# Kernel optimization log

Hardware: AMD Instinct MI355X
Metric: run time of the kernel (lower is better)

The kernel has to match this reference:

```python
import jax, jax.numpy as jnp
import numpy as np

N = 262144      # total nodes
G = 256         # graphs
P = 1024        # nodes per graph (k=None sort pool keeps all)
E = 4194304     # edges
F_IN = 128
H = 32
C = 10          # out capsules / classes
OUT_LEN = 16
IN_LEN = 96     # 3 * 32 concat
NUM_ITERS = 3


def setup_inputs() -> dict:
    key = jax.random.key(0)
    ks = jax.random.split(key, 12)
    x = jax.random.normal(ks[0], (N, F_IN), jnp.float32)
    # edges within each graph of size P
    src = jax.random.randint(ks[1], (E,), 0, N)
    off = jax.random.randint(ks[2], (E,), 0, P)
    dst = (src // P) * P + off
    edge_index = jnp.stack([src, dst]).astype(jnp.int64)
    batch = jnp.repeat(jnp.arange(G), P).astype(jnp.int64)
    W1 = jax.random.normal(ks[3], (F_IN, H), jnp.float32) / np.sqrt(F_IN)
    b1 = jnp.zeros((H,), jnp.float32)
    W2 = jax.random.normal(ks[4], (H, H), jnp.float32) / np.sqrt(H)
    b2 = jnp.zeros((H,), jnp.float32)
    W3 = jax.random.normal(ks[5], (H, H), jnp.float32) / np.sqrt(H)
    b3 = jnp.zeros((H,), jnp.float32)
    caps_W = jax.random.normal(ks[6], (C, OUT_LEN, IN_LEN), jnp.float32) * 0.05
    return {"x": x, "edge_index": edge_index, "batch": batch,
            "W1": W1, "b1": b1, "W2": W2, "b2": b2, "W3": W3, "b3": b3,
            "caps_W": caps_W}


def _position_encoding(length, dim):
    pos = jnp.arange(length, dtype=jnp.float32)[:, None]
    i = jnp.arange(dim // 2, dtype=jnp.float32)[None, :]
    ang = pos / jnp.power(10000.0, 2.0 * i / dim)
    return jnp.stack([jnp.sin(ang), jnp.cos(ang)], axis=-1).reshape(length, dim)


def _squash(v, eps=1e-12):
    n2 = jnp.sum(v * v, axis=-1, keepdims=True)
    return (n2 / (1.0 + n2)) * v / jnp.sqrt(n2 + eps)


def reference(x, edge_index, batch, W1, b1, W2, b2, W3, b3, caps_W):
    src, dst = edge_index[0], edge_index[1]
    # remove_self_loops, then GCNConv re-adds self loops with weight 1
    mask = (src != dst).astype(x.dtype)
    deg = jax.ops.segment_sum(mask, dst, num_segments=N) + 1.0
    dis = jax.lax.rsqrt(deg)                         # deg^{-1/2}
    enorm = dis[src] * dis[dst] * mask               # [E]

    def gcn(h, W, b):
        h = h @ W                                    # [N,H]
        agg = jax.ops.segment_sum(h[src] * enorm[:, None], dst, num_segments=N)
        agg = agg + h * (dis * dis)[:, None]         # self-loop term deg^{-1}
        return jnp.tanh(agg + b)

    x1 = gcn(x, W1, b1)
    x2 = gcn(x1, W2, b2)
    x3 = gcn(x2, W3, b3)
    h = jnp.concatenate([x1, x2, x3], axis=-1)       # [N, 96]

    # global_sort_pool (k=None): per-graph sort by last channel, descending
    hg = h.reshape(G, P, IN_LEN)
    order = jnp.argsort(-hg[:, :, -1], axis=1)
    hs = jnp.take_along_axis(hg, order[:, :, None], axis=1)  # [G,P,96]
    hs = hs + _position_encoding(P, IN_LEN)[None]

    # CapsuleLinear, shared weight: priors [G, C, P, OUT_LEN]
    priors = jnp.einsum('oji,gki->gokj', caps_W, hs)

    # k-means routing
    v = jnp.mean(priors, axis=2, keepdims=True)      # [G,C,1,OUT_LEN]
    for _ in range(NUM_ITERS):
        vn = v / (jnp.linalg.norm(v, axis=-1, keepdims=True) + 1e-12)
        logits = jnp.sum(priors * vn, axis=-1, keepdims=True)  # [G,C,P,1]
        prob = jax.nn.softmax(logits, axis=2)
        v = jnp.sum(prob * priors, axis=2, keepdims=True)
    out = _squash(v)[:, :, 0, :]                     # [G, C, OUT_LEN]
    return jnp.linalg.norm(out, axis=-1)             # [G, C]
```

## Files before the change

### kernel.cpp

```cpp
#include <hip/hip_runtime.h>
#include <hip/hip_fp16.h>
#include <cstdint>
#include <cstddef>

#define N_NODES   262144
#define NG        256
#define PP        1024
#define NE        4194304
#define FIN       128
#define HH        32
#define NC        10
#define OL        16
#define IL        96
#define NITER     3
#define ECHUNK    4096
#define NCHUNK    (NE/ECHUNK)
#define ECAP      18432
#define HSTR      36

typedef _Float16 half8 __attribute__((ext_vector_type(8)));
typedef float f32x4 __attribute__((ext_vector_type(4)));

__global__ void k_hist(const int* __restrict__ ei, unsigned* __restrict__ histT) {
  __shared__ unsigned lh[NG];
  int t = threadIdx.x, b = blockIdx.x;
  lh[t] = 0;
  __syncthreads();
  int base = b * ECHUNK;
  for (int q = t; q < ECHUNK; q += 256) {
    int e = base + q;
    int s = ei[e], d = ei[NE + e];
    if (s != d) atomicAdd(&lh[s >> 10], 1u);
  }
  __syncthreads();
  histT[t * NCHUNK + b] = lh[t];
}

__global__ void k_scanA(const unsigned* __restrict__ histT, unsigned* __restrict__ cbaseT,
                        unsigned* __restrict__ gtot) {
  __shared__ unsigned wtot[4];
  int t = threadIdx.x, g = blockIdx.x;
  int lane = t & 63, wv = t >> 6;
  uint4 hv = *(const uint4*)(histT + (size_t)g * NCHUNK + t * 4);
  unsigned s0 = hv.x, s1 = s0 + hv.y, s2 = s1 + hv.z, s3 = s2 + hv.w;
  unsigned tsum = s3, sc = tsum;
  for (int d = 1; d < 64; d <<= 1) {
    unsigned v = __shfl_up(sc, d, 64);
    if (lane >= d) sc += v;
  }
  if (lane == 63) wtot[wv] = sc;
  __syncthreads();
  unsigned woff = 0;
  for (int w = 0; w < wv; ++w) woff += wtot[w];
  unsigned base = woff + sc - tsum;
  cbaseT[(size_t)(t * 4 + 0) * NG + g] = base;
  cbaseT[(size_t)(t * 4 + 1) * NG + g] = base + s0;
  cbaseT[(size_t)(t * 4 + 2) * NG + g] = base + s1;
  cbaseT[(size_t)(t * 4 + 3) * NG + g] = base + s2;
  if (t == 255) gtot[g] = woff + sc;
}

__global__ void k_scanB(const unsigned* __restrict__ gtot, unsigned* __restrict__ gbase) {
  __shared__ unsigned wtot[4];
  int t = threadIdx.x;
  int lane = t & 63, wv = t >> 6;
  unsigned x = gtot[t], sc = x;
  for (int d = 1; d < 64; d <<= 1) {
    unsigned v = __shfl_up(sc, d, 64);
    if (lane >= d) sc += v;
  }
  if (lane == 63) wtot[wv] = sc;
  __syncthreads();
  unsigned woff = 0;
  for (int w = 0; w < wv; ++w) woff += wtot[w];
  gbase[t] = woff + sc - x;
  if (t == 255) gbase[256] = woff + sc;
}

__global__ void k_scatter(const int* __restrict__ ei, const unsigned* __restrict__ cbaseT,
                          const unsigned* __restrict__ gbase, unsigned* __restrict__ epack) {
  __shared__ unsigned lcur[NG];
  int t = threadIdx.x, b = blockIdx.x;
  lcur[t] = gbase[t] + cbaseT[(size_t)b * NG + t];
  __syncthreads();
  int base = b * ECHUNK;
  for (int q = t; q < ECHUNK; q += 256) {
    int e = base + q;
    int s = ei[e], d = ei[NE + e];
    if (s != d) {
      int g = s >> 10;
      unsigned pos = atomicAdd(&lcur[g], 1u);
      epack[pos] = (unsigned)(s & 1023) | ((unsigned)(d & 1023) << 10);
    }
  }
}

__global__ __launch_bounds__(256) void k_dstsort(const unsigned* __restrict__ epack,
                          const unsigned* __restrict__ gbase,
                          unsigned short* __restrict__ esrc16,
                          unsigned* __restrict__ dstptr) {
  __shared__ unsigned shist[PP];
  __shared__ unsigned wsum[256];
  __shared__ unsigned cur[PP];
  int t = threadIdx.x, g = blockIdx.x;
  unsigned e0 = gbase[g], e1 = gbase[g + 1];
  for (int i = t; i < PP; i += 256) shist[i] = 0;
  __syncthreads();
  for (unsigned e = e0 + t; e < e1; e += 256)
    atomicAdd(&shist[(epack[e] >> 10) & 1023], 1u);
  __syncthreads();
  unsigned h0 = shist[4 * t], h1 = shist[4 * t + 1], h2 = shist[4 * t + 2], h3 = shist[4 * t + 3];
  unsigned tsum = h0 + h1 + h2 + h3;
  wsum[t] = tsum;
  __syncthreads();
  for (int off = 1; off < 256; off <<= 1) {
    unsigned v = (t >= off) ? wsum[t - off] : 0u;
    __syncthreads();
    wsum[t] += v;
    __syncthreads();
  }
  unsigned excl = wsum[t] - tsum;
  unsigned c0 = excl, c1 = c0 + h0, c2 = c1 + h1, c3 = c2 + h2;
  cur[4 * t] = c0; cur[4 * t + 1] = c1; cur[4 * t + 2] = c2; cur[4 * t + 3] = c3;
  unsigned* dp = dstptr + (size_t)g * (PP + 1);
  dp[4 * t] = c0; dp[4 * t + 1] = c1; dp[4 * t + 2] = c2; dp[4 * t + 3] = c3;
  if (t == 0) dp[PP] = e1 - e0;
  __syncthreads();
  unsigned short* eg = esrc16 + (size_t)g * ECAP;
  for (unsigned e = e0 + t; e < e1; e += 256) {
    unsigned pk = epack[e];
    unsigned so = pk & 1023, dofs = (pk >> 10) & 1023;
    unsigned pos = atomicAdd(&cur[dofs], 1u);
    if (pos < ECAP) eg[pos] = (unsigned short)so;
  }
}

__global__ void k_dis(const unsigned* __restrict__ dstptr, float* __restrict__ dis) {
  int n = blockIdx.x * 256 + threadIdx.x;
  int g = n >> 10, k = n & 1023;
  const unsigned* dp = dstptr + (size_t)g * (PP + 1) + k;
  float deg = (float)(dp[1] - dp[0]);
  dis[n] = 1.0f / sqrtf(deg + 1.0f);
}

__device__ __forceinline__ void gcn_layer(float* hsl, const float* dg, const unsigned* dp,
                                          const unsigned short* eg, const float* bias,
                                          int coloff, const float* Wn, float* hbase, int t) {
  float4 bl[8];
#pragma unroll
  for (int j = 0; j < 8; ++j) bl[j] = ((const float4*)bias)[j];
  if (Wn) {
#pragma unroll
    for (int pp = 0; pp < 8; ++pp) {
      int p = t + pp * 512;
      hsl[(p >> 2) * HSTR + 32 + (p & 3)] = Wn[p];
    }
  }
  float xn[2][32];
#pragma unroll
  for (int pth = 0; pth < 2; ++pth) {
    int k = t + pth * 512;
    float dk = dg[k];
    unsigned e0 = dp[k], e1 = dp[k + 1];
    if (e1 > (unsigned)ECAP) e1 = ECAP;
    float4 acc[8];
    const float* sp = &hsl[k * HSTR];
#pragma unroll
    for (int j = 0; j < 8; ++j) acc[j] = *(const float4*)(sp + 4 * j);
    unsigned e = e0;
    for (; e + 1 < e1; e += 2) {
      int s0 = eg[e], s1 = eg[e + 1];
      const float* q0 = &hsl[s0 * HSTR];
      const float* q1 = &hsl[s1 * HSTR];
#pragma unroll
      for (int j = 0; j < 8; ++j) {
        float4 a = *(const float4*)(q0 + 4 * j);
        float4 b2 = *(const float4*)(q1 + 4 * j);
        acc[j].x += a.x + b2.x; acc[j].y += a.y + b2.y;
        acc[j].z += a.z + b2.z; acc[j].w += a.w + b2.w;
      }
    }
    if (e < e1) {
      int s0 = eg[e];
      const float* q0 = &hsl[s0 * HSTR];
#pragma unroll
      for (int j = 0; j < 8; ++j) {
        float4 a = *(const float4*)(q0 + 4 * j);
        acc[j].x += a.x; acc[j].y += a.y; acc[j].z += a.z; acc[j].w += a.w;
      }
    }
#pragma unroll
    for (int j = 0; j < 8; ++j) {
      xn[pth][4 * j + 0] = tanhf(dk * acc[j].x + bl[j].x);
      xn[pth][4 * j + 1] = tanhf(dk * acc[j].y + bl[j].y);
      xn[pth][4 * j + 2] = tanhf(dk * acc[j].z + bl[j].z);
      xn[pth][4 * j + 3] = tanhf(dk * acc[j].w + bl[j].w);
    }
    float* hr = hbase + (size_t)k * IL + coloff;
#pragma unroll
    for (int j = 0; j < 8; ++j) {
      float4 s;
      s.x = xn[pth][4 * j]; s.y = xn[pth][4 * j + 1];
      s.z = xn[pth][4 * j + 2]; s.w = xn[pth][4 * j + 3];
      *(float4*)(hr + 4 * j) = s;
    }
  }
  __syncthreads();
  if (Wn) {
#pragma unroll
    for (int pth = 0; pth < 2; ++pth) {
      int k = t + pth * 512;
      float dk = dg[k];
      float4 o4[8];
#pragma unroll
      for (int j = 0; j < 8; ++j) { o4[j].x = 0.f; o4[j].y = 0.f; o4[j].z = 0.f; o4[j].w = 0.f; }
#pragma unroll
      for (int c = 0; c < 32; ++c) {
        float xc = xn[pth][c];
#pragma unroll
        for (int j4 = 0; j4 < 8; ++j4) {
          float4 w = *(const float4*)&hsl[(c * 8 + j4) * HSTR + 32];
          o4[j4].x += xc * w.x; o4[j4].y += xc * w.y;
          o4[j4].z += xc * w.z; o4[j4].w += xc * w.w;
        }
      }
      float* op = &hsl[k * HSTR];
#pragma unroll
      for (int j4 = 0; j4 < 8; ++j4) {
        float4 s;
        s.x = o4[j4].x * dk; s.y = o4[j4].y * dk;
        s.z = o4[j4].z * dk; s.w = o4[j4].w * dk;
        *(float4*)(op + 4 * j4) = s;
      }
    }
    __syncthreads();
  }
}

__global__ __launch_bounds__(512) void k_gcn(const float* __restrict__ x,
                                             const float* __restrict__ dis,
                                             const unsigned short* __restrict__ esrc16,
                                             const unsigned* __restrict__ dstptr,
                                             const float* __restrict__ W1, const float* __restrict__ b1,
                                             const float* __restrict__ W2, const float* __restrict__ b2,
                                             const float* __restrict__ W3, const float* __restrict__ b3,
                                             float* __restrict__ h) {
  __shared__ float hsl[PP * HSTR];
  int t = threadIdx.x, g = blockIdx.x;
  const float* dg = dis + (size_t)g * PP;
  const unsigned* dp = dstptr + (size_t)g * (PP + 1);
  const unsigned short* eg = esrc16 + (size_t)g * ECAP;
  float* hbase = h + (size_t)g * PP * IL;

#pragma unroll
  for (int pp = 0; pp < 8; ++pp) {
    int p = t + pp * 512;
    hsl[(p >> 2) * HSTR + 32 + (p & 3)] = W1[p];
  }
  __syncthreads();

  {
    int cg = t & 3, ng = t >> 2;
    int row0 = ng * 8;
    const float* xr = x + ((size_t)g * PP + row0) * FIN;
    float acc[8][8];
#pragma unroll
    for (int r = 0; r < 8; ++r)
#pragma unroll
      for (int j = 0; j < 8; ++j) acc[r][j] = 0.f;
    for (int k4 = 0; k4 < FIN / 4; ++k4) {
      float4 xv[8];
#pragma unroll
      for (int r = 0; r < 8; ++r)
        xv[r] = *(const float4*)(xr + (size_t)r * FIN + k4 * 4);
#pragma unroll
      for (int kk = 0; kk < 4; ++kk) {
        int k = k4 * 4 + kk;
        float4 wa = *(const float4*)&hsl[(k * 8 + cg * 2) * HSTR + 32];
        float4 wb = *(const float4*)&hsl[(k * 8 + cg * 2 + 1) * HSTR + 32];
#pragma unroll
        for (int r = 0; r < 8; ++r) {
          float xk = kk == 0 ? xv[r].x : kk == 1 ? xv[r].y : kk == 2 ? xv[r].z : xv[r].w;
          acc[r][0] += xk * wa.x; acc[r][1] += xk * wa.y;
          acc[r][2] += xk * wa.z; acc[r][3] += xk * wa.w;
          acc[r][4] += xk * wb.x; acc[r][5] += xk * wb.y;
          acc[r][6] += xk * wb.z; acc[r][7] += xk * wb.w;
        }
      }
    }
#pragma unroll
    for (int r = 0; r < 8; ++r) {
      float d = dg[row0 + r];
      float4 s0, s1;
      s0.x = acc[r][0] * d; s0.y = acc[r][1] * d; s0.z = acc[r][2] * d; s0.w = acc[r][3] * d;
      s1.x = acc[r][4] * d; s1.y = acc[r][5] * d; s1.z = acc[r][6] * d; s1.w = acc[r][7] * d;
      *(float4*)&hsl[(row0 + r) * HSTR + cg * 8] = s0;
      *(float4*)&hsl[(row0 + r) * HSTR + cg * 8 + 4] = s1;
    }
  }
  __syncthreads();

  gcn_layer(hsl, dg, dp, eg, b1, 0,  W2, hbase, t);
  gcn_layer(hsl, dg, dp, eg, b2, 32, W3, hbase, t);
  gcn_layer(hsl, dg, dp, eg, b3, 64, nullptr, hbase, t);
}

__global__ __launch_bounds__(512) void k_sort(const float* __restrict__ h,
                                              unsigned short* __restrict__ rank16) {
  __shared__ float key[PP];
  __shared__ unsigned sidx[PP];
  int t = threadIdx.x, g = blockIdx.x;
  for (int i = t; i < PP; i += 512) {
    key[i] = h[(size_t)(g * PP + i) * IL + (IL - 1)];
    sidx[i] = i;
  }
  __syncthreads();
  for (int sz = 2; sz <= PP; sz <<= 1) {
    for (int st = sz >> 1; st > 0; st >>= 1) {
      int i = 2 * t - (t & (st - 1));
      int j = i + st;
      float ki = key[i], kj = key[j];
      unsigned ii = sidx[i], ij = sidx[j];
      bool less_ji = (kj > ki) || (kj == ki && ij < ii);
      bool asc = ((i & sz) == 0);
      if (less_ji == asc) { key[i] = kj; key[j] = ki; sidx[i] = ij; sidx[j] = ii; }
      __syncthreads();
    }
  }
  for (int i = t; i < PP; i += 512) rank16[g * PP + sidx[i]] = (unsigned short)i;
}

__global__ void k_pe(float* __restrict__ pe) {
  int id = blockIdx.x * 256 + threadIdx.x;
  if (id >= PP * 48) return;
  int pos = id / 48, i = id % 48;
  float denom = powf(10000.0f, (2.0f * i) / 96.0f);
  float ang = (float)pos / denom;
  pe[pos * IL + 2 * i] = sinf(ang);
  pe[pos * IL + 2 * i + 1] = cosf(ang);
}

__global__ void k_wpe(const float* __restrict__ pe, const float* __restrict__ capsW,
                      __half* __restrict__ wpe) {
  int id = blockIdx.x * 256 + threadIdx.x;
  if (id >= NC * PP * OL) return;
  int j = id & 15;
  int pos = (id >> 4) & 1023;
  int c = id >> 14;
  const float* wr = capsW + (size_t)(c * OL + j) * IL;
  const float* pr = pe + (size_t)pos * IL;
  float a = 0;
#pragma unroll 8
  for (int i = 0; i < IL; ++i) a += wr[i] * pr[i];
  wpe[(((size_t)c << 10) + pos) * 16 + j] = __float2half(a);
}

__global__ __launch_bounds__(256) void k_pgemm(const float* __restrict__ h,
                                               const float* __restrict__ capsW,
                                               __half* __restrict__ Pc) {
  int t = threadIdx.x, b = blockIdx.x;
  int g = b >> 2;
  int wv = t >> 6, lane = t & 63;
  int quad = lane >> 4, l16 = lane & 15;
  half8 afr[4][3];
#pragma unroll
  for (int rt = 0; rt < 4; ++rt) {
    int row = b * 256 + wv * 64 + rt * 16 + l16;
    const float* hr = h + (size_t)row * IL + quad * 8;
#pragma unroll
    for (int kb = 0; kb < 3; ++kb) {
      float4 x = *(const float4*)(hr + kb * 32);
      float4 y = *(const float4*)(hr + kb * 32 + 4);
      half8 a;
      a[0] = (_Float16)x.x; a[1] = (_Float16)x.y; a[2] = (_Float16)x.z; a[3] = (_Float16)x.w;
      a[4] = (_Float16)y.x; a[5] = (_Float16)y.y; a[6] = (_Float16)y.z; a[7] = (_Float16)y.w;
      afr[rt][kb] = a;
    }
  }
  int krow_base = (b & 3) * 256 + wv * 64;
  for (int ct = 0; ct < NC; ++ct) {
    half8 bfr[3];
    const float* wr = capsW + (size_t)(ct * 16 + l16) * IL + quad * 8;
#pragma unroll
    for (int kb = 0; kb < 3; ++kb) {
      float4 x = *(const float4*)(wr + kb * 32);
      float4 y = *(const float4*)(wr + kb * 32 + 4);
      half8 bb;
      bb[0] = (_Float16)x.x; bb[1] = (_Float16)x.y; bb[2] = (_Float16)x.z; bb[3] = (_Float16)x.w;
      bb[4] = (_Float16)y.x; bb[5] = (_Float16)y.y; bb[6] = (_Float16)y.z; bb[7] = (_Float16)y.w;
      bfr[kb] = bb;
    }
#pragma unroll
    for (int rt = 0; rt < 4; ++rt) {
      f32x4 acc = {0.f, 0.f, 0.f, 0.f};
      acc = __builtin_amdgcn_mfma_f32_16x16x32_f16(afr[rt][0], bfr[0], acc, 0, 0, 0);
      acc = __builtin_amdgcn_mfma_f32_16x16x32_f16(afr[rt][1], bfr[1], acc, 0, 0, 0);
      acc = __builtin_amdgcn_mfma_f32_16x16x32_f16(afr[rt][2], bfr[2], acc, 0, 0, 0);
      int krow = krow_base + rt * 16;
      __half* po = Pc + ((((size_t)g * NC + ct) << 10) + krow) * 16 + l16;
#pragma unroll
      for (int r = 0; r < 4; ++r)
        po[(quad * 4 + r) * 16] = __float2half(acc[r]);
    }
  }
}

__global__ __launch_bounds__(256) void k_route2(const __half* __restrict__ Pc,
                                                const __half* __restrict__ wpe,
                                                const unsigned short* __restrict__ rank16,
                                                float* __restrict__ out) {
  __shared__ float v_l[16];
  __shared__ float wred[4][17];
  int t = threadIdx.x;
  int gc = blockIdx.x;
  int g = gc / NC, c = gc - g * NC;
  int lane = t & 63, wv = t >> 6;
  const __half* pg = Pc + ((size_t)gc << 10) * 16;
  const unsigned short* rk = rank16 + (size_t)g * PP;
  const __half* wc = wpe + ((size_t)c << 10) * 16;
  float pr[4][16];
  float vsum[16];
#pragma unroll
  for (int i = 0; i < 16; ++i) vsum[i] = 0.f;
#pragma unroll
  for (int r = 0; r < 4; ++r) {
    int k = t + r * 256;
    uint4 a0 = *(const uint4*)(pg + (size_t)k * 16);
    uint4 a1 = *(const uint4*)(pg + (size_t)k * 16 + 8);
    int rkk = rk[k];
    uint4 b0 = *(const uint4*)(wc + (size_t)rkk * 16);
    uint4 b1 = *(const uint4*)(wc + (size_t)rkk * 16 + 8);
    const __half2* pa0 = (const __half2*)&a0; const __half2* pa1 = (const __half2*)&a1;
    const __half2* pb0 = (const __half2*)&b0; const __half2* pb1 = (const __half2*)&b1;
#pragma unroll
    for (int j = 0; j < 4; ++j) {
      float2 fa = __half22float2(pa0[j]); float2 fb = __half22float2(pb0[j]);
      pr[r][2 * j] = fa.x + fb.x; pr[r][2 * j + 1] = fa.y + fb.y;
      float2 fa1 = __half22float2(pa1[j]); float2 fb1 = __half22float2(pb1[j]);
      pr[r][8 + 2 * j] = fa1.x + fb1.x; pr[r][8 + 2 * j + 1] = fa1.y + fb1.y;
    }
#pragma unroll
    for (int i = 0; i < 16; ++i) vsum[i] += pr[r][i];
  }
#pragma unroll
  for (int d = 1; d < 64; d <<= 1)
#pragma unroll
    for (int i = 0; i < 16; ++i) vsum[i] += __shfl_xor(vsum[i], d, 64);
  if (lane == 0) {
#pragma unroll
    for (int i = 0; i < 16; ++i) wred[wv][i] = vsum[i];
  }
  __syncthreads();
  if (t < 16) v_l[t] = wred[0][t] + wred[1][t] + wred[2][t] + wred[3][t];
  __syncthreads();
  for (int it = 0; it < NITER; ++it) {
    float vn[16]; float n2 = 0;
#pragma unroll
    for (int i = 0; i < 16; ++i) { float x = v_l[i]; vn[i] = x; n2 += x * x; }
    float inv = 1.0f / (sqrtf(n2) + 1e-12f);
#pragma unroll
    for (int i = 0; i < 16; ++i) vn[i] *= inv;
    float lg[4];
#pragma unroll
    for (int r = 0; r < 4; ++r) {
      float a = 0;
#pragma unroll
      for (int i = 0; i < 16; ++i) a += pr[r][i] * vn[i];
      lg[r] = a;
    }
    float mx = fmaxf(fmaxf(lg[0], lg[1]), fmaxf(lg[2], lg[3]));
#pragma unroll
    for (int d = 1; d < 64; d <<= 1) mx = fmaxf(mx, __shfl_xor(mx, d, 64));
    __syncthreads();
    if (lane == 0) wred[wv][16] = mx;
    __syncthreads();
    float gmax = fmaxf(fmaxf(wred[0][16], wred[1][16]), fmaxf(wred[2][16], wred[3][16]));
    float es = 0; float eacc[16];
#pragma unroll
    for (int i = 0; i < 16; ++i) eacc[i] = 0.f;
#pragma unroll
    for (int r = 0; r < 4; ++r) {
      float e = __expf(lg[r] - gmax);
      es += e;
#pragma unroll
      for (int i = 0; i < 16; ++i) eacc[i] += e * pr[r][i];
    }
#pragma unroll
    for (int d = 1; d < 64; d <<= 1) {
      es += __shfl_xor(es, d, 64);
#pragma unroll
      for (int i = 0; i < 16; ++i) eacc[i] += __shfl_xor(eacc[i], d, 64);
    }
    __syncthreads();
    if (lane == 0) {
#pragma unroll
      for (int i = 0; i < 16; ++i) wred[wv][i] = eacc[i];
      wred[wv][16] = es;
    }
    __syncthreads();
    if (t < 16) {
      float s = wred[0][t] + wred[1][t] + wred[2][t] + wred[3][t];
      float S = wred[0][16] + wred[1][16] + wred[2][16] + wred[3][16];
      v_l[t] = s / S;
    }
    __syncthreads();
  }
  if (t == 0) {
    float n2 = 0;
#pragma unroll
    for (int i = 0; i < 16; ++i) { float x = v_l[i]; n2 += x * x; }
    out[gc] = (n2 / (1.0f + n2)) * sqrtf(n2) / sqrtf(n2 + 1e-12f);
  }
}

extern "C" void kernel_launch(void* const* d_in, const int* in_sizes, int n_in,
                              void* d_out, int out_size, void* d_ws, size_t ws_size,
                              hipStream_t stream) {
  const float* x     = (const float*)d_in[0];
  const int*   ei    = (const int*)d_in[1];
  const float* W1    = (const float*)d_in[3];
  const float* b1    = (const float*)d_in[4];
  const float* W2    = (const float*)d_in[5];
  const float* b2    = (const float*)d_in[6];
  const float* W3    = (const float*)d_in[7];
  const float* b3    = (const float*)d_in[8];
  const float* capsW = (const float*)d_in[9];
  float* out = (float*)d_out;

  char* wp = (char*)d_ws;
  auto alloc = [&](size_t bytes) { char* p = wp; wp += (bytes + 255) & ~(size_t)255; return p; };
  float*    dis    = (float*)alloc((size_t)N_NODES * 4);
  float*    h      = (float*)alloc((size_t)N_NODES * IL * 4);
  char*     ureg   = wp;
  unsigned* epack  = (unsigned*)alloc((size_t)NE * 4);
  unsigned short* esrc16 = (unsigned short*)alloc((size_t)NG * ECAP * 2);
  unsigned* histT  = (unsigned*)alloc((size_t)NCHUNK * NG * 4);
  unsigned* cbaseT = (unsigned*)alloc((size_t)NCHUNK * NG * 4);
  const size_t PC_BYTES = (size_t)NG * NC * PP * 16 * 2;
  if ((size_t)(wp - ureg) < PC_BYTES) wp = ureg + ((PC_BYTES + 255) & ~(size_t)255);
  __half*   Pc     = (__half*)ureg;
  unsigned* gtot   = (unsigned*)alloc((size_t)NG * 4);
  unsigned* gbase  = (unsigned*)alloc((size_t)(NG + 1) * 4);
  unsigned* dstptr = (unsigned*)alloc((size_t)NG * (PP + 1) * 4);
  unsigned short* rank16 = (unsigned short*)alloc((size_t)NG * PP * 2);
  float*    pe     = (float*)alloc((size_t)PP * IL * 4);
  __half*   wpe    = (__half*)alloc((size_t)NC * PP * OL * 2);

  k_hist<<<NCHUNK, 256, 0, stream>>>(ei, histT);
  k_scanA<<<NG, 256, 0, stream>>>(histT, cbaseT, gtot);
  k_scanB<<<1, 256, 0, stream>>>(gtot, gbase);
  k_scatter<<<NCHUNK, 256, 0, stream>>>(ei, cbaseT, gbase, epack);
  k_dstsort<<<NG, 256, 0, stream>>>(epack, gbase, esrc16, dstptr);
  k_dis<<<N_NODES / 256, 256, 0, stream>>>(dstptr, dis);
  k_pe<<<(PP * 48) / 256, 256, 0, stream>>>(pe);
  k_wpe<<<(NC * PP * OL) / 256, 256, 0, stream>>>(pe, capsW, wpe);

  k_gcn<<<NG, 512, 0, stream>>>(x, dis, esrc16, dstptr, W1, b1, W2, b2, W3, b3, h);

  k_sort<<<NG, 512, 0, stream>>>(h, rank16);
  k_pgemm<<<N_NODES / 256, 256, 0, stream>>>(h, capsW, Pc);
  k_route2<<<NG * NC, 256, 0, stream>>>(Pc, wpe, rank16, out);
}
```

Measured before the change: 628.6 us.

## Fuse capsule GEMM with routing, store GCN output in fp16, fast tanh

The GCN kernel now writes concatenated features as fp16 and stores the sort key separately. It uses an exp-based tanh and reads the next layer's weights straight from global memory instead of staging them in LDS. The separate priors GEMM and routing kernels are merged into one per-graph kernel that keeps priors in LDS and loops over the 10 capsules, so the fp16 priors buffer never goes through HBM. The trade-offs are fp16 rounding of the features, lower per-block parallelism in the merged kernel (256 blocks looping over capsules with many block syncs), and extra global weight reads in the GCN.

New measurement: 656.6 us. 1.04x slower.

```diff
diff --git a/kernel.cpp b/kernel.cpp
--- a/kernel.cpp
+++ b/kernel.cpp
@@ -17,9 +17,19 @@
 #define NCHUNK    (NE/ECHUNK)
 #define ECAP      18432
 #define HSTR      36
+#define PLSTR     20
 
 typedef _Float16 half8 __attribute__((ext_vector_type(8)));
 typedef float f32x4 __attribute__((ext_vector_type(4)));
+
+__device__ __forceinline__ float tanh_fast(float x) {
+  float e = __expf(2.0f * x);
+  return 1.0f - 2.0f / (e + 1.0f);
+}
+__device__ __forceinline__ unsigned pk2(float a, float b) {
+  __half2 h = __floats2half2_rn(a, b);
+  return *reinterpret_cast<unsigned*>(&h);
+}
 
 __global__ void k_hist(const int* __restrict__ ei, unsigned* __restrict__ histT) {
   __shared__ unsigned lh[NG];
@@ -145,17 +155,11 @@
 
 __device__ __forceinline__ void gcn_layer(float* hsl, const float* dg, const unsigned* dp,
                                           const unsigned short* eg, const float* bias,
-                                          int coloff, const float* Wn, float* hbase, int t) {
+                                          int coloff, const float* Wn, __half* hb16,
+                                          float* keyArr, int t) {
   float4 bl[8];
 #pragma unroll
   for (int j = 0; j < 8; ++j) bl[j] = ((const float4*)bias)[j];
-  if (Wn) {
-#pragma unroll
-    for (int pp = 0; pp < 8; ++pp) {
-      int p = t + pp * 512;
-      hsl[(p >> 2) * HSTR + 32 + (p & 3)] = Wn[p];
-    }
-  }
   float xn[2][32];
 #pragma unroll
   for (int pth = 0; pth < 2; ++pth) {
@@ -191,19 +195,22 @@
     }
 #pragma unroll
     for (int j = 0; j < 8; ++j) {
-      xn[pth][4 * j + 0] = tanhf(dk * acc[j].x + bl[j].x);
-      xn[pth][4 * j + 1] = tanhf(dk * acc[j].y + bl[j].y);
-      xn[pth][4 * j + 2] = tanhf(dk * acc[j].z + bl[j].z);
-      xn[pth][4 * j + 3] = tanhf(dk * acc[j].w + bl[j].w);
-    }
-    float* hr = hbase + (size_t)k * IL + coloff;
-#pragma unroll
-    for (int j = 0; j < 8; ++j) {
-      float4 s;
-      s.x = xn[pth][4 * j]; s.y = xn[pth][4 * j + 1];
-      s.z = xn[pth][4 * j + 2]; s.w = xn[pth][4 * j + 3];
-      *(float4*)(hr + 4 * j) = s;
-    }
+      xn[pth][4 * j + 0] = tanh_fast(dk * acc[j].x + bl[j].x);
+      xn[pth][4 * j + 1] = tanh_fast(dk * acc[j].y + bl[j].y);
+      xn[pth][4 * j + 2] = tanh_fast(dk * acc[j].z + bl[j].z);
+      xn[pth][4 * j + 3] = tanh_fast(dk * acc[j].w + bl[j].w);
+    }
+    __half* hr = hb16 + (size_t)k * IL + coloff;
+#pragma unroll
+    for (int j4 = 0; j4 < 4; ++j4) {
+      uint4 u;
+      u.x = pk2(xn[pth][8 * j4 + 0], xn[pth][8 * j4 + 1]);
+      u.y = pk2(xn[pth][8 * j4 + 2], xn[pth][8 * j4 + 3]);
+      u.z = pk2(xn[pth][8 * j4 + 4], xn[pth][8 * j4 + 5]);
+      u.w = pk2(xn[pth][8 * j4 + 6], xn[pth][8 * j4 + 7]);
+      *(uint4*)(hr + 8 * j4) = u;
+    }
+    if (keyArr) keyArr[k] = xn[pth][31];
   }
   __syncthreads();
   if (Wn) {
@@ -217,9 +224,10 @@
 #pragma unroll
       for (int c = 0; c < 32; ++c) {
         float xc = xn[pth][c];
+        const float4* wr = (const float4*)(Wn + c * 32);
 #pragma unroll
         for (int j4 = 0; j4 < 8; ++j4) {
-          float4 w = *(const float4*)&hsl[(c * 8 + j4) * HSTR + 32];
+          float4 w = wr[j4];
           o4[j4].x += xc * w.x; o4[j4].y += xc * w.y;
           o4[j4].z += xc * w.z; o4[j4].w += xc * w.w;
         }
@@ -237,20 +245,21 @@
   }
 }
 
-__global__ __launch_bounds__(512) void k_gcn(const float* __restrict__ x,
+__global__ __launch_bounds__(512, 1) void k_gcn(const float* __restrict__ x,
                                              const float* __restrict__ dis,
                                              const unsigned short* __restrict__ esrc16,
                                              const unsigned* __restrict__ dstptr,
                                              const float* __restrict__ W1, const float* __restrict__ b1,
                                              const float* __restrict__ W2, const float* __restrict__ b2,
                                              const float* __restrict__ W3, const float* __restrict__ b3,
-                                             float* __restrict__ h) {
+                                             __half* __restrict__ h16, float* __restrict__ key) {
   __shared__ float hsl[PP * HSTR];
   int t = threadIdx.x, g = blockIdx.x;
   const float* dg = dis + (size_t)g * PP;
   const unsigned* dp = dstptr + (size_t)g * (PP + 1);
   const unsigned short* eg = esrc16 + (size_t)g * ECAP;
-  float* hbase = h + (size_t)g * PP * IL;
+  __half* hb16 = h16 + (size_t)g * PP * IL;
+  float* keyg = key + (size_t)g * PP;
 
 #pragma unroll
   for (int pp = 0; pp < 8; ++pp) {
@@ -300,18 +309,18 @@
   }
   __syncthreads();
 
-  gcn_layer(hsl, dg, dp, eg, b1, 0,  W2, hbase, t);
-  gcn_layer(hsl, dg, dp, eg, b2, 32, W3, hbase, t);
-  gcn_layer(hsl, dg, dp, eg, b3, 64, nullptr, hbase, t);
-}
-
-__global__ __launch_bounds__(512) void k_sort(const float* __restrict__ h,
+  gcn_layer(hsl, dg, dp, eg, b1, 0,  W2, hb16, nullptr, t);
+  gcn_layer(hsl, dg, dp, eg, b2, 32, W3, hb16, nullptr, t);
+  gcn_layer(hsl, dg, dp, eg, b3, 64, nullptr, hb16, keyg, t);
+}
+
+__global__ __launch_bounds__(512) void k_sort(const float* __restrict__ keyArr,
                                               unsigned short* __restrict__ rank16) {
   __shared__ float key[PP];
   __shared__ unsigned sidx[PP];
   int t = threadIdx.x, g = blockIdx.x;
   for (int i = t; i < PP; i += 512) {
-    key[i] = h[(size_t)(g * PP + i) * IL + (IL - 1)];
+    key[i] = keyArr[(size_t)g * PP + i];
     sidx[i] = i;
   }
   __syncthreads();
@@ -355,161 +364,162 @@
   wpe[(((size_t)c << 10) + pos) * 16 + j] = __float2half(a);
 }
 
-__global__ __launch_bounds__(256) void k_pgemm(const float* __restrict__ h,
-                                               const float* __restrict__ capsW,
-                                               __half* __restrict__ Pc) {
-  int t = threadIdx.x, b = blockIdx.x;
-  int g = b >> 2;
+__global__ __launch_bounds__(512, 1) void k_caps(const __half* __restrict__ h16,
+                                                 const float* __restrict__ capsW,
+                                                 const __half* __restrict__ wpe,
+                                                 const unsigned short* __restrict__ rank16,
+                                                 float* __restrict__ out) {
+  __shared__ float pls[PP * PLSTR];
+  __shared__ float wred[8][17];
+  __shared__ float v_l[16];
+  int t = threadIdx.x, g = blockIdx.x;
   int wv = t >> 6, lane = t & 63;
   int quad = lane >> 4, l16 = lane & 15;
-  half8 afr[4][3];
-#pragma unroll
-  for (int rt = 0; rt < 4; ++rt) {
-    int row = b * 256 + wv * 64 + rt * 16 + l16;
-    const float* hr = h + (size_t)row * IL + quad * 8;
+  const __half* hg = h16 + (size_t)g * PP * IL;
+  const unsigned short* rk = rank16 + (size_t)g * PP;
+
+  half8 afr[8][3];
+#pragma unroll
+  for (int rt = 0; rt < 8; ++rt) {
+    int row = wv * 128 + rt * 16 + l16;
+    const char* hr = (const char*)(hg + (size_t)row * IL);
 #pragma unroll
     for (int kb = 0; kb < 3; ++kb) {
-      float4 x = *(const float4*)(hr + kb * 32);
-      float4 y = *(const float4*)(hr + kb * 32 + 4);
-      half8 a;
-      a[0] = (_Float16)x.x; a[1] = (_Float16)x.y; a[2] = (_Float16)x.z; a[3] = (_Float16)x.w;
-      a[4] = (_Float16)y.x; a[5] = (_Float16)y.y; a[6] = (_Float16)y.z; a[7] = (_Float16)y.w;
-      afr[rt][kb] = a;
-    }
-  }
-  int krow_base = (b & 3) * 256 + wv * 64;
+      uint4 u = *(const uint4*)(hr + kb * 64 + quad * 16);
+      afr[rt][kb] = *(half8*)&u;
+    }
+  }
+  int k0 = t, k1 = t + 512;
+  int rk0 = rk[k0], rk1 = rk[k1];
+
   for (int ct = 0; ct < NC; ++ct) {
     half8 bfr[3];
     const float* wr = capsW + (size_t)(ct * 16 + l16) * IL + quad * 8;
 #pragma unroll
     for (int kb = 0; kb < 3; ++kb) {
-      float4 x = *(const float4*)(wr + kb * 32);
-      float4 y = *(const float4*)(wr + kb * 32 + 4);
+      float4 xx = *(const float4*)(wr + kb * 32);
+      float4 yy = *(const float4*)(wr + kb * 32 + 4);
       half8 bb;
-      bb[0] = (_Float16)x.x; bb[1] = (_Float16)x.y; bb[2] = (_Float16)x.z; bb[3] = (_Float16)x.w;
-      bb[4] = (_Float16)y.x; bb[5] = (_Float16)y.y; bb[6] = (_Float16)y.z; bb[7] = (_Float16)y.w;
+      bb[0] = (_Float16)xx.x; bb[1] = (_Float16)xx.y; bb[2] = (_Float16)xx.z; bb[3] = (_Float16)xx.w;
+      bb[4] = (_Float16)yy.x; bb[5] = (_Float16)yy.y; bb[6] = (_Float16)yy.z; bb[7] = (_Float16)yy.w;
       bfr[kb] = bb;
     }
 #pragma unroll
-    for (int rt = 0; rt < 4; ++rt) {
+    for (int rt = 0; rt < 8; ++rt) {
       f32x4 acc = {0.f, 0.f, 0.f, 0.f};
       acc = __builtin_amdgcn_mfma_f32_16x16x32_f16(afr[rt][0], bfr[0], acc, 0, 0, 0);
       acc = __builtin_amdgcn_mfma_f32_16x16x32_f16(afr[rt][1], bfr[1], acc, 0, 0, 0);
       acc = __builtin_amdgcn_mfma_f32_16x16x32_f16(afr[rt][2], bfr[2], acc, 0, 0, 0);
-      int krow = krow_base + rt * 16;
-      __half* po = Pc + ((((size_t)g * NC + ct) << 10) + krow) * 16 + l16;
+      int rbase = wv * 128 + rt * 16 + quad * 4;
 #pragma unroll
       for (int r = 0; r < 4; ++r)
-        po[(quad * 4 + r) * 16] = __float2half(acc[r]);
-    }
-  }
-}
-
-__global__ __launch_bounds__(256) void k_route2(const __half* __restrict__ Pc,
-                                                const __half* __restrict__ wpe,
-                                                const unsigned short* __restrict__ rank16,
-                                                float* __restrict__ out) {
-  __shared__ float v_l[16];
-  __shared__ float wred[4][17];
-  int t = threadIdx.x;
-  int gc = blockIdx.x;
-  int g = gc / NC, c = gc - g * NC;
-  int lane = t & 63, wv = t >> 6;
-  const __half* pg = Pc + ((size_t)gc << 10) * 16;
-  const unsigned short* rk = rank16 + (size_t)g * PP;
-  const __half* wc = wpe + ((size_t)c << 10) * 16;
-  float pr[4][16];
-  float vsum[16];
-#pragma unroll
-  for (int i = 0; i < 16; ++i) vsum[i] = 0.f;
-#pragma unroll
-  for (int r = 0; r < 4; ++r) {
-    int k = t + r * 256;
-    uint4 a0 = *(const uint4*)(pg + (size_t)k * 16);
-    uint4 a1 = *(const uint4*)(pg + (size_t)k * 16 + 8);
-    int rkk = rk[k];
-    uint4 b0 = *(const uint4*)(wc + (size_t)rkk * 16);
-    uint4 b1 = *(const uint4*)(wc + (size_t)rkk * 16 + 8);
-    const __half2* pa0 = (const __half2*)&a0; const __half2* pa1 = (const __half2*)&a1;
-    const __half2* pb0 = (const __half2*)&b0; const __half2* pb1 = (const __half2*)&b1;
-#pragma unroll
-    for (int j = 0; j < 4; ++j) {
-      float2 fa = __half22float2(pa0[j]); float2 fb = __half22float2(pb0[j]);
-      pr[r][2 * j] = fa.x + fb.x; pr[r][2 * j + 1] = fa.y + fb.y;
-      float2 fa1 = __half22float2(pa1[j]); float2 fb1 = __half22float2(pb1[j]);
-      pr[r][8 + 2 * j] = fa1.x + fb1.x; pr[r][8 + 2 * j + 1] = fa1.y + fb1.y;
-    }
-#pragma unroll
-    for (int i = 0; i < 16; ++i) vsum[i] += pr[r][i];
-  }
-#pragma unroll
-  for (int d = 1; d < 64; d <<= 1)
-#pragma unroll
-    for (int i = 0; i < 16; ++i) vsum[i] += __shfl_xor(vsum[i], d, 64);
-  if (lane == 0) {
-#pragma unroll
-    for (int i = 0; i < 16; ++i) wred[wv][i] = vsum[i];
-  }
-  __syncthreads();
-  if (t < 16) v_l[t] = wred[0][t] + wred[1][t] + wred[2][t] + wred[3][t];
-  __syncthreads();
-  for (int it = 0; it < NITER; ++it) {
-    float vn[16]; float n2 = 0;
-#pragma unroll
-    for (int i = 0; i < 16; ++i) { float x = v_l[i]; vn[i] = x; n2 += x * x; }
-    float inv = 1.0f / (sqrtf(n2) + 1e-12f);
-#pragma unroll
-    for (int i = 0; i < 16; ++i) vn[i] *= inv;
-    float lg[4];
-#pragma unroll
-    for (int r = 0; r < 4; ++r) {
-      float a = 0;
-#pragma unroll
-      for (int i = 0; i < 16; ++i) a += pr[r][i] * vn[i];
-      lg[r] = a;
-    }
-    float mx = fmaxf(fmaxf(lg[0], lg[1]), fmaxf(lg[2], lg[3]));
-#pragma unroll
-    for (int d = 1; d < 64; d <<= 1) mx = fmaxf(mx, __shfl_xor(mx, d, 64));
-    __syncthreads();
-    if (lane == 0) wred[wv][16] = mx;
-    __syncthreads();
-    float gmax = fmaxf(fmaxf(wred[0][16], wred[1][16]), fmaxf(wred[2][16], wred[3][16]));
-    float es = 0; float eacc[16];
-#pragma unroll
-    for (int i = 0; i < 16; ++i) eacc[i] = 0.f;
-#pragma unroll
-    for (int r = 0; r < 4; ++r) {
-      float e = __expf(lg[r] - gmax);
-      es += e;
-#pragma unroll
-      for (int i = 0; i < 16; ++i) eacc[i] += e * pr[r][i];
-    }
-#pragma unroll
-    for (int d = 1; d < 64; d <<= 1) {
-      es += __shfl_xor(es, d, 64);
-#pragma unroll
-      for (int i = 0; i < 16; ++i) eacc[i] += __shfl_xor(eacc[i], d, 64);
-    }
-    __syncthreads();
+        pls[(rbase + r) * PLSTR + l16] = acc[r];
+    }
+    __syncthreads();
+
+    float pr[2][16];
+#pragma unroll
+    for (int i = 0; i < 2; ++i) {
+      int k = i == 0 ? k0 : k1;
+      int rkk = i == 0 ? rk0 : rk1;
+      const float* pp = &pls[k * PLSTR];
+      const __half* wc = wpe + (((size_t)ct << 10) + rkk) * 16;
+      uint4 w0 = *(const uint4*)wc;
+      uint4 w1 = *(const uint4*)(wc + 8);
+      const __half2* pw0 = (const __half2*)&w0;
+      const __half2* pw1 = (const __half2*)&w1;
+#pragma unroll
+      for (int j = 0; j < 4; ++j) {
+        float2 f0 = __half22float2(pw0[j]);
+        float2 f1 = __half22float2(pw1[j]);
+        pr[i][2 * j] = pp[2 * j] + f0.x;
+        pr[i][2 * j + 1] = pp[2 * j + 1] + f0.y;
+        pr[i][8 + 2 * j] = pp[8 + 2 * j] + f1.x;
+        pr[i][8 + 2 * j + 1] = pp[8 + 2 * j + 1] + f1.y;
+      }
+    }
+    float vsum[16];
+#pragma unroll
+    for (int i = 0; i < 16; ++i) vsum[i] = pr[0][i] + pr[1][i];
+#pragma unroll
+    for (int d = 1; d < 64; d <<= 1)
+#pragma unroll
+      for (int i = 0; i < 16; ++i) vsum[i] += __shfl_xor(vsum[i], d, 64);
     if (lane == 0) {
 #pragma unroll
-      for (int i = 0; i < 16; ++i) wred[wv][i] = eacc[i];
-      wred[wv][16] = es;
+      for (int i = 0; i < 16; ++i) wred[wv][i] = vsum[i];
     }
     __syncthreads();
     if (t < 16) {
-      float s = wred[0][t] + wred[1][t] + wred[2][t] + wred[3][t];
-      float S = wred[0][16] + wred[1][16] + wred[2][16] + wred[3][16];
-      v_l[t] = s / S;
-    }
-    __syncthreads();
-  }
-  if (t == 0) {
-    float n2 = 0;
-#pragma unroll
-    for (int i = 0; i < 16; ++i) { float x = v_l[i]; n2 += x * x; }
-    out[gc] = (n2 / (1.0f + n2)) * sqrtf(n2) / sqrtf(n2 + 1e-12f);
+      float s = 0;
+#pragma unroll
+      for (int w = 0; w < 8; ++w) s += wred[w][t];
+      v_l[t] = s;
+    }
+    __syncthreads();
+
+    for (int it = 0; it < NITER; ++it) {
+      float vn[16]; float n2 = 0;
+#pragma unroll
+      for (int i = 0; i < 16; ++i) { float xv = v_l[i]; vn[i] = xv; n2 += xv * xv; }
+      float inv = 1.0f / (sqrtf(n2) + 1e-12f);
+#pragma unroll
+      for (int i = 0; i < 16; ++i) vn[i] *= inv;
+      float lg[2];
+#pragma unroll
+      for (int i = 0; i < 2; ++i) {
+        float a = 0;
+#pragma unroll
+        for (int j = 0; j < 16; ++j) a += pr[i][j] * vn[j];
+        lg[i] = a;
+      }
+      float mx = fmaxf(lg[0], lg[1]);
+#pragma unroll
+      for (int d = 1; d < 64; d <<= 1) mx = fmaxf(mx, __shfl_xor(mx, d, 64));
+      __syncthreads();
+      if (lane == 0) wred[wv][16] = mx;
+      __syncthreads();
+      float gmax = wred[0][16];
+#pragma unroll
+      for (int w = 1; w < 8; ++w) gmax = fmaxf(gmax, wred[w][16]);
+      float es = 0; float eacc[16];
+#pragma unroll
+      for (int i = 0; i < 16; ++i) eacc[i] = 0.f;
+#pragma unroll
+      for (int i = 0; i < 2; ++i) {
+        float e = __expf(lg[i] - gmax);
+        es += e;
+#pragma unroll
+        for (int j = 0; j < 16; ++j) eacc[j] += e * pr[i][j];
+      }
+#pragma unroll
+      for (int d = 1; d < 64; d <<= 1) {
+        es += __shfl_xor(es, d, 64);
+#pragma unroll
+        for (int i = 0; i < 16; ++i) eacc[i] += __shfl_xor(eacc[i], d, 64);
+      }
+      __syncthreads();
+      if (lane == 0) {
+#pragma unroll
+        for (int i = 0; i < 16; ++i) wred[wv][i] = eacc[i];
+        wred[wv][16] = es;
+      }
+      __syncthreads();
+      if (t < 16) {
+        float s = 0, S = 0;
+#pragma unroll
+        for (int w = 0; w < 8; ++w) { s += wred[w][t]; S += wred[w][16]; }
+        v_l[t] = s / S;
+      }
+      __syncthreads();
+    }
+    if (t == 0) {
+      float n2 = 0;
+#pragma unroll
+      for (int i = 0; i < 16; ++i) { float xv = v_l[i]; n2 += xv * xv; }
+      out[g * NC + ct] = (n2 / (1.0f + n2)) * sqrtf(n2) / sqrtf(n2 + 1e-12f);
+    }
+    __syncthreads();
   }
 }
 
@@ -530,15 +540,12 @@
   char* wp = (char*)d_ws;
   auto alloc = [&](size_t bytes) { char* p = wp; wp += (bytes + 255) & ~(size_t)255; return p; };
   float*    dis    = (float*)alloc((size_t)N_NODES * 4);
-  float*    h      = (float*)alloc((size_t)N_NODES * IL * 4);
-  char*     ureg   = wp;
+  __half*   h16    = (__half*)alloc((size_t)N_NODES * IL * 2);
+  float*    key    = (float*)alloc((size_t)N_NODES * 4);
   unsigned* epack  = (unsigned*)alloc((size_t)NE * 4);
   unsigned short* esrc16 = (unsigned short*)alloc((size_t)NG * ECAP * 2);
   unsigned* histT  = (unsigned*)alloc((size_t)NCHUNK * NG * 4);
   unsigned* cbaseT = (unsigned*)alloc((size_t)NCHUNK * NG * 4);
-  const size_t PC_BYTES = (size_t)NG * NC * PP * 16 * 2;
-  if ((size_t)(wp - ureg) < PC_BYTES) wp = ureg + ((PC_BYTES + 255) & ~(size_t)255);
-  __half*   Pc     = (__half*)ureg;
   unsigned* gtot   = (unsigned*)alloc((size_t)NG * 4);
   unsigned* gbase  = (unsigned*)alloc((size_t)(NG + 1) * 4);
   unsigned* dstptr = (unsigned*)alloc((size_t)NG * (PP + 1) * 4);
@@ -555,9 +562,8 @@
   k_pe<<<(PP * 48) / 256, 256, 0, stream>>>(pe);
   k_wpe<<<(NC * PP * OL) / 256, 256, 0, stream>>>(pe, capsW, wpe);
 
-  k_gcn<<<NG, 512, 0, stream>>>(x, dis, esrc16, dstptr, W1, b1, W2, b2, W3, b3, h);
-
-  k_sort<<<NG, 512, 0, stream>>>(h, rank16);
-  k_pgemm<<<N_NODES / 256, 256, 0, stream>>>(h, capsW, Pc);
-  k_route2<<<NG * NC, 256, 0, stream>>>(Pc, wpe, rank16, out);
-}
+  k_gcn<<<NG, 512, 0, stream>>>(x, dis, esrc16, dstptr, W1, b1, W2, b2, W3, b3, h16, key);
+
+  k_sort<<<NG, 512, 0, stream>>>(key, rank16);
+  k_caps<<<NG, 512, 0, stream>>>(h16, capsW, wpe, rank16, out);
+}
```
